# Optimization experiments

Measured on AMD Instinct MI355X. Metric: run time of the kernel, lower is better.

## Reference

```python
import math
import jax, jax.numpy as jnp
import numpy as np

HEADS = 8
DIM_HEAD = 32
DIM = 128
EPS_LN = 1e-5
EPS_NORM = 1e-12


def setup_inputs() -> dict:
    key = jax.random.key(0)
    ks = jax.random.split(key, 4)
    inner = HEADS * DIM_HEAD  # 256
    x = jax.random.normal(ks[0], (1, DIM, 16, 64, 64), dtype=jnp.float32)
    g = jnp.ones((1, DIM, 1, 1, 1), dtype=jnp.float32)
    b = jnp.zeros((1, DIM, 1, 1, 1), dtype=jnp.float32)
    w_qkv = jax.random.normal(ks[1], (3 * inner, DIM), dtype=jnp.float32) * 0.05
    w_out = jax.random.normal(ks[2], (DIM, inner), dtype=jnp.float32) * 0.05
    b_out = jnp.zeros((DIM,), dtype=jnp.float32)
    return {"x": x, "g": g, "b": b, "w_qkv": w_qkv, "w_out": w_out, "b_out": b_out}


def _l2norm_ch(t):
    # F.normalize(t, dim=1): divide by max(||t||_2, eps) along channel axis
    n = jnp.sqrt(jnp.sum(t * t, axis=1, keepdims=True))
    return t / jnp.maximum(n, EPS_NORM)


def _gather_axis(t, idx, axis):
    # t: [bh, c, D, H, W]; idx: [bh, kk]; gather along spatial `axis`
    shape = list(t.shape)
    shape[axis] = idx.shape[1]
    ix = idx.reshape((idx.shape[0],) + (1,) * (axis - 1) + (idx.shape[1],) + (1,) * (4 - axis))
    ix = jnp.broadcast_to(ix, shape)
    return jnp.take_along_axis(t, ix, axis=axis)


def _dpsa_forward(x, g, b, w_qkv, w_out, b_out):
    bsz, c, D, H, W = x.shape
    kd = int(math.ceil(D ** 0.5))
    kh = int(math.ceil(H ** 0.5))
    kw = int(math.ceil(W ** 0.5))

    # ChanLayerNorm3d (biased variance over channel dim)
    mean = jnp.mean(x, axis=1, keepdims=True)
    var = jnp.var(x, axis=1, keepdims=True)
    xn = (x - mean) / jnp.sqrt(var + EPS_LN) * g + b

    # 1x1x1 conv to qkv (no bias)
    qkv = jnp.einsum('oc,bcdhw->bodhw', w_qkv, xn)
    inner = HEADS * DIM_HEAD
    q, k, v = qkv[:, :inner], qkv[:, inner:2 * inner], qkv[:, 2 * inner:]

    def fold(t):  # b (i c) d h w -> (b i) c d h w
        return t.reshape(bsz * HEADS, DIM_HEAD, D, H, W)
    q, k, v = fold(q), fold(k), fold(v)
    D0, H0, W0 = D, H, W

    q = _l2norm_ch(q)
    k = _l2norm_ch(k)
    q_abs = jnp.abs(q)

    # depth pruning
    if kd < D:
        q_probe = q_abs.sum(axis=(3, 4))                 # [bh, c, D]
        k_probe = jnp.abs(k).sum(axis=(3, 4))            # [bh, c, D]
        score = jnp.einsum('bcd,bcd->bd', q_probe, k_probe)
        _, idx = jax.lax.top_k(score, kd)
        k = _gather_axis(k, idx, 2)
        v = _gather_axis(v, idx, 2)
        D = kd
    # height pruning
    if kh < H:
        q_probe = q_abs.sum(axis=(2, 4))                 # [bh, c, H]
        k_probe = jnp.abs(k).sum(axis=(2, 4))            # [bh, c, H]
        score = jnp.einsum('bch,bch->bh', q_probe, k_probe)
        _, idx = jax.lax.top_k(score, kh)
        k = _gather_axis(k, idx, 3)
        v = _gather_axis(v, idx, 3)
        H = kh
    # width pruning
    if kw < W:
        q_probe = q_abs.sum(axis=(2, 3))                 # [bh, c, W]
        k_probe = jnp.abs(k).sum(axis=(2, 3))            # [bh, c, W]
        score = jnp.einsum('bcw,bcw->bw', q_probe, k_probe)
        _, idx = jax.lax.top_k(score, kw)
        k = _gather_axis(k, idx, 4)
        v = _gather_axis(v, idx, 4)
        W = kw

    def flat(t):  # b c d h w -> b (dhw) c
        return t.reshape(t.shape[0], t.shape[1], -1).transpose(0, 2, 1)
    qf, kf, vf = flat(q), flat(k), flat(v)

    sim = jnp.einsum('bic,bjc->bij', qf, kf)  # note: original applies no scale
    attn = jax.nn.softmax(sim, axis=-1)
    out_flat = jnp.einsum('bij,bjc->bic', attn, vf)  # [bh, N, c]

    # faithful to torch .view: raw row-major reinterpretation
    out = out_flat.reshape(bsz * HEADS, DIM_HEAD, D0, H0, W0)
    out = out.reshape(bsz, HEADS * DIM_HEAD, D0, H0, W0)
    return jnp.einsum('oc,bcdhw->bodhw', w_out, out) + b_out[None, :, None, None, None]


def reference(x, g, b, w_qkv, w_out, b_out):
    return _dpsa_forward(x, g, b, w_qkv, w_out, b_out)
```

## Files before the change

### kernel.cpp

```cpp
#include <hip/hip_runtime.h>
#include <math.h>

#define P_TOT 65536
#define CH    128
#define NHEAD 8
#define KD    4
#define KH    8
#define KW    8
#define NJ    256

typedef unsigned short u16;
typedef unsigned int   u32;
typedef __attribute__((ext_vector_type(8))) short frag8;
typedef __attribute__((ext_vector_type(4))) float f32x4;

__device__ inline u16 bf16r(float a) {
    u32 ua = __float_as_uint(a);
    return (u16)((ua + 0x7fff + ((ua >> 16) & 1)) >> 16);
}
__device__ inline float bf16f(u16 h) {
    return __uint_as_float(((u32)h) << 16);
}
__device__ inline u32 packhl(float v) {
    u16 hh = bf16r(v);
    u16 ll = bf16r(v - bf16f(hh));
    return (u32)hh | ((u32)ll << 16);
}

__global__ __launch_bounds__(256) void k_ln(const float* __restrict__ x,
                                            const float* __restrict__ g,
                                            const float* __restrict__ b,
                                            u16* __restrict__ xn_hi,
                                            u16* __restrict__ xn_lo) {
    __shared__ u32 buf[64 * 131];
    __shared__ float red[8 * 64];
    __shared__ float stat[2 * 64];
    float* xt = (float*)buf;
    int t  = threadIdx.x;
    int p0 = blockIdx.x * 64;
    #pragma unroll
    for (int r = 0; r < 8; ++r) {
        int id = t + 256 * r;
        int c = id >> 4, q4 = id & 15;
        *(float4*)(xt + c * 64 + q4 * 4) =
            *(const float4*)(x + (size_t)c * P_TOT + p0 + q4 * 4);
    }
    __syncthreads();
    int pp = t & 63, part = t >> 6;
    float sum = 0.f, ssq = 0.f;
    for (int ci = 0; ci < 32; ++ci) {
        float v = xt[(part * 32 + ci) * 64 + pp];
        sum += v; ssq += v * v;
    }
    red[part * 64 + pp] = sum;
    red[256 + part * 64 + pp] = ssq;
    __syncthreads();
    if (t < 64) {
        float s = red[t] + red[64 + t] + red[128 + t] + red[192 + t];
        float q = red[256 + t] + red[320 + t] + red[384 + t] + red[448 + t];
        float mean = s * (1.f / CH);
        float var  = q * (1.f / CH) - mean * mean;
        stat[t] = mean;
        stat[64 + t] = 1.f / sqrtf(var + 1e-5f);
    }
    __syncthreads();
    float mean = stat[pp], inv = stat[64 + pp];
    u32 pk[32];
    for (int ci = 0; ci < 32; ++ci) {
        int c = part * 32 + ci;
        float v  = xt[c * 64 + pp];
        float xn = (v - mean) * inv * g[c] + b[c];
        pk[ci] = packhl(xn);
    }
    __syncthreads();
    u32* tr = buf;
    for (int ci = 0; ci < 32; ++ci)
        tr[pp * 131 + part * 32 + ci] = pk[ci];
    __syncthreads();
    #pragma unroll
    for (int r = 0; r < 8; ++r) {
        int id = t + 256 * r;
        int pr = id >> 5, ch = id & 31;
        const u32* srcp = tr + pr * 131 + ch * 4;
        u32 v0 = srcp[0], v1 = srcp[1], v2 = srcp[2], v3 = srcp[3];
        uint2 hv, lv;
        hv.x = __builtin_amdgcn_perm(v1, v0, 0x05040100);
        hv.y = __builtin_amdgcn_perm(v3, v2, 0x05040100);
        lv.x = __builtin_amdgcn_perm(v1, v0, 0x07060302);
        lv.y = __builtin_amdgcn_perm(v3, v2, 0x07060302);
        size_t off = (size_t)(p0 + pr) * 128 + ch * 4;
        *(uint2*)(xn_hi + off) = hv;
        *(uint2*)(xn_lo + off) = lv;
    }
}

__global__ __launch_bounds__(256) void k_wsplit(const float* __restrict__ wqkv,
                                                const float* __restrict__ wout,
                                                u16* __restrict__ w_hi,
                                                u16* __restrict__ w_lo,
                                                u16* __restrict__ w2_hi,
                                                u16* __restrict__ w2_lo,
                                                float* __restrict__ zbuf) {
    int id = blockIdx.x * 256 + threadIdx.x;
    if (id < 40960) zbuf[id] = 0.f;
    if (id < 65536) {
        float v = wqkv[id];
        u16 hh = bf16r(v);
        w_hi[id] = hh; w_lo[id] = bf16r(v - bf16f(hh));
    } else {
        int j = id - 65536;
        float v = wout[j];
        u16 hh = bf16r(v);
        w2_hi[j] = hh; w2_lo[j] = bf16r(v - bf16f(hh));
    }
}

__global__ __launch_bounds__(256) void k_gemm_qkv(const u16* __restrict__ xn_hi,
                                                  const u16* __restrict__ xn_lo,
                                                  const u16* __restrict__ w_hi,
                                                  const u16* __restrict__ w_lo,
                                                  float* __restrict__ qk,
                                                  u16* __restrict__ qT,
                                                  float* __restrict__ pd,
                                                  float* __restrict__ pdh,
                                                  float* __restrict__ qph,
                                                  float* __restrict__ qpw) {
    __shared__ u16 smem[4 * 128 * 64];
    u16* a_hi = smem;
    u16* a_lo = smem + 8192;
    u16* b_hi = smem + 16384;
    u16* b_lo = smem + 24576;
    int t    = threadIdx.x;
    int lane = t & 63, wave = t >> 6;
    int wp = wave & 1, wo = wave >> 1;
    int m = lane & 15, quad = lane >> 4;
    int p0 = blockIdx.x * 128;
    int o0 = blockIdx.y * 128;
    f32x4 acc[4][4] = {};
    for (int k0 = 0; k0 < 128; k0 += 64) {
        __syncthreads();
        #pragma unroll
        for (int r = 0; r < 4; ++r) {
            int id  = t + 256 * r;
            int row = id >> 3, gg = id & 7;
            int gs  = gg ^ (row & 7);
            int dst = row * 64 + gg * 8;
            size_t sa = (size_t)(p0 + row) * 128 + k0 + gs * 8;
            size_t sb = (size_t)(o0 + row) * 128 + k0 + gs * 8;
            *(uint4*)(a_hi + dst) = *(const uint4*)(xn_hi + sa);
            *(uint4*)(a_lo + dst) = *(const uint4*)(xn_lo + sa);
            *(uint4*)(b_hi + dst) = *(const uint4*)(w_hi + sb);
            *(uint4*)(b_lo + dst) = *(const uint4*)(w_lo + sb);
        }
        __syncthreads();
        #pragma unroll
        for (int ks = 0; ks < 2; ++ks) {
            frag8 ah[4], al[4], bh[4], bl[4];
            #pragma unroll
            for (int i = 0; i < 4; ++i) {
                int row = wp * 64 + i * 16 + m;
                int gg  = (ks * 4 + quad) ^ (row & 7);
                ah[i] = *(const frag8*)(a_hi + row * 64 + gg * 8);
                al[i] = *(const frag8*)(a_lo + row * 64 + gg * 8);
            }
            #pragma unroll
            for (int j = 0; j < 4; ++j) {
                int row = wo * 64 + j * 16 + m;
                int gg  = (ks * 4 + quad) ^ (row & 7);
                bh[j] = *(const frag8*)(b_hi + row * 64 + gg * 8);
                bl[j] = *(const frag8*)(b_lo + row * 64 + gg * 8);
            }
            #pragma unroll
            for (int i = 0; i < 4; ++i)
                #pragma unroll
                for (int j = 0; j < 4; ++j) {
                    acc[i][j] = __builtin_amdgcn_mfma_f32_16x16x32_bf16(ah[i], bh[j], acc[i][j], 0, 0, 0);
                    acc[i][j] = __builtin_amdgcn_mfma_f32_16x16x32_bf16(ah[i], bl[j], acc[i][j], 0, 0, 0);
                    acc[i][j] = __builtin_amdgcn_mfma_f32_16x16x32_bf16(al[i], bh[j], acc[i][j], 0, 0, 0);
                }
        }
    }
    #pragma unroll
    for (int i = 0; i < 4; ++i) {
        #pragma unroll
        for (int jg = 0; jg < 2; ++jg) {
            f32x4 s;
            #pragma unroll
            for (int r = 0; r < 4; ++r)
                s[r] = acc[i][2 * jg][r] * acc[i][2 * jg][r]
                     + acc[i][2 * jg + 1][r] * acc[i][2 * jg + 1][r];
            #pragma unroll
            for (int mask = 1; mask <= 8; mask <<= 1) {
                s[0] += __shfl_xor(s[0], mask, 64);
                s[1] += __shfl_xor(s[1], mask, 64);
                s[2] += __shfl_xor(s[2], mask, 64);
                s[3] += __shfl_xor(s[3], mask, 64);
            }
            #pragma unroll
            for (int r = 0; r < 4; ++r) {
                float inv = 1.f / fmaxf(sqrtf(s[r]), 1e-12f);
                acc[i][2 * jg][r]     *= inv;
                acc[i][2 * jg + 1][r] *= inv;
            }
        }
    }
    int pb = blockIdx.x;
    int d  = pb >> 5;
    int hh = (2 * pb + wp) & 63;
    bool isQ = (o0 < 256);
    {
        float sj[4];
        #pragma unroll
        for (int j = 0; j < 4; ++j) {
            float s = 0.f;
            #pragma unroll
            for (int i = 0; i < 4; ++i)
                #pragma unroll
                for (int r = 0; r < 4; ++r)
                    s += fabsf(acc[i][j][r]);
            sj[j] = s;
        }
        #pragma unroll
        for (int j = 0; j < 4; ++j) {
            sj[j] += __shfl_xor(sj[j], 16, 64);
            sj[j] += __shfl_xor(sj[j], 32, 64);
        }
        if (quad == 0) {
            #pragma unroll
            for (int j = 0; j < 4; ++j) {
                int o = o0 + wo * 64 + j * 16 + m;
                atomicAdd(pd + o * 16 + d, sj[j]);
                if (isQ) atomicAdd(qph + o * 64 + hh, sj[j]);
                else     pdh[((size_t)o * 16 + d) * 64 + hh] = sj[j];
            }
        }
    }
    if (isQ) {
        float* qw = (float*)smem;
        __syncthreads();
        if (wp == 0) {
            #pragma unroll
            for (int j = 0; j < 4; ++j) {
                int ol = wo * 64 + j * 16 + m;
                #pragma unroll
                for (int i = 0; i < 4; ++i)
                    #pragma unroll
                    for (int r = 0; r < 4; ++r)
                        qw[(i * 16 + quad * 4 + r) * 132 + ol] = fabsf(acc[i][j][r]);
            }
        }
        __syncthreads();
        if (wp == 1) {
            #pragma unroll
            for (int j = 0; j < 4; ++j) {
                int ol = wo * 64 + j * 16 + m;
                #pragma unroll
                for (int i = 0; i < 4; ++i)
                    #pragma unroll
                    for (int r = 0; r < 4; ++r)
                        qw[(i * 16 + quad * 4 + r) * 132 + ol] += fabsf(acc[i][j][r]);
            }
        }
        __syncthreads();
        #pragma unroll
        for (int ri = 0; ri < 32; ++ri) {
            int id = t + 256 * ri;
            int ol = id >> 6, w = id & 63;
            atomicAdd(qpw + (size_t)(o0 + ol) * 64 + w, qw[w * 132 + ol]);
        }
    } else {
        #pragma unroll
        for (int i = 0; i < 4; ++i) {
            int p = p0 + wp * 64 + i * 16 + quad * 4;
            #pragma unroll
            for (int j = 0; j < 4; ++j) {
                int o = o0 + wo * 64 + j * 16 + m;
                float4 v;
                v.x = acc[i][j][0]; v.y = acc[i][j][1];
                v.z = acc[i][j][2]; v.w = acc[i][j][3];
                *(float4*)(qk + (size_t)o * P_TOT + p) = v;
            }
        }
    }
    if (isQ) {
        __syncthreads();
        u16* qtb = smem;
        #pragma unroll
        for (int i = 0; i < 4; ++i)
            #pragma unroll
            for (int j = 0; j < 4; ++j) {
                int grp = wo * 2 + (j >> 1);
                int c   = (j & 1) * 16 + m;
                #pragma unroll
                for (int r = 0; r < 4; ++r) {
                    int pl = wp * 64 + i * 16 + quad * 4 + r;
                    qtb[grp * 5120 + pl * 40 + c] = bf16r(acc[i][j][r]);
                }
            }
        __syncthreads();
        int gbase = o0 >> 5;
        #pragma unroll
        for (int ri = 0; ri < 8; ++ri) {
            int id = t + 256 * ri;
            int grp = id >> 9, rem = id & 511;
            int pl = rem >> 2, cq = rem & 3;
            uint4 v = *(const uint4*)(qtb + grp * 5120 + pl * 40 + cq * 8);
            *(uint4*)(qT + ((size_t)(gbase + grp) * P_TOT + p0 + pl) * 32 + cq * 8) = v;
        }
    }
}

__global__ __launch_bounds__(64) void k_topk_d(const float* __restrict__ pd,
                                               int* __restrict__ idx_d) {
    int h = blockIdx.x, t = threadIdx.x;
    __shared__ float sc[16];
    if (t < 16) {
        float s = 0.f;
        for (int c = 0; c < 32; ++c)
            s += pd[(h * 32 + c) * 16 + t] * pd[(256 + h * 32 + c) * 16 + t];
        sc[t] = s;
    }
    __syncthreads();
    if (t == 0) {
        bool used[16] = {};
        for (int r = 0; r < KD; ++r) {
            int best = 0; float bv = -1e30f;
            for (int i = 0; i < 16; ++i)
                if (!used[i] && sc[i] > bv) { bv = sc[i]; best = i; }
            used[best] = true;
            idx_d[h * KD + r] = best;
        }
    }
}

__global__ __launch_bounds__(256) void k_topk_h(const float* __restrict__ qph,
                                                const float* __restrict__ pdh,
                                                const int* __restrict__ idx_d,
                                                int* __restrict__ idx_h) {
    int h = blockIdx.x, t = threadIdx.x;
    int tq = t & 63, cg = t >> 6;
    __shared__ float sc2[4][64];
    __shared__ float sc[64];
    int ds[KD];
    #pragma unroll
    for (int i = 0; i < KD; ++i) ds[i] = idx_d[h * KD + i];
    float partial = 0.f;
    for (int ci = 0; ci < 8; ++ci) {
        int c  = cg * 8 + ci;
        int oq = h * 32 + c, ok = 256 + h * 32 + c;
        float qp = qph[oq * 64 + tq];
        float kp = 0.f;
        #pragma unroll
        for (int i = 0; i < KD; ++i) kp += pdh[(ok * 16 + ds[i]) * 64 + tq];
        partial += qp * kp;
    }
    sc2[cg][tq] = partial;
    __syncthreads();
    if (t < 64) sc[t] = sc2[0][t] + sc2[1][t] + sc2[2][t] + sc2[3][t];
    __syncthreads();
    if (t == 0) {
        bool used[64] = {};
        for (int r = 0; r < KH; ++r) {
            int best = 0; float bv = -1e30f;
            for (int i = 0; i < 64; ++i)
                if (!used[i] && sc[i] > bv) { bv = sc[i]; best = i; }
            used[best] = true;
            idx_h[h * KH + r] = best;
        }
    }
}

__global__ __launch_bounds__(64) void k_probe_w(const float* __restrict__ qk,
                                                const int* __restrict__ idx_d,
                                                const int* __restrict__ idx_h,
                                                float* __restrict__ kpw) {
    int o2 = blockIdx.x;
    int w  = threadIdx.x;
    int h  = o2 >> 5;
    const float* src = qk + (256 + o2) * P_TOT;
    float s = 0.f;
    for (int i = 0; i < KD; ++i) {
        int pb = idx_d[h * KD + i] * 4096;
        for (int j = 0; j < KH; ++j)
            s += fabsf(src[pb + idx_h[h * KH + j] * 64 + w]);
    }
    kpw[o2 * 64 + w] = s;
}

__global__ __launch_bounds__(256) void k_topk_w(const float* __restrict__ qpw,
                                                const float* __restrict__ kpw,
                                                int* __restrict__ idx_w) {
    int h = blockIdx.x, t = threadIdx.x;
    int tq = t & 63, cg = t >> 6;
    __shared__ float sc2[4][64];
    __shared__ float sc[64];
    float partial = 0.f;
    for (int ci = 0; ci < 8; ++ci) {
        int c  = cg * 8 + ci;
        int oq = h * 32 + c;
        partial += qpw[oq * 64 + tq] * kpw[(h * 32 + c) * 64 + tq];
    }
    sc2[cg][tq] = partial;
    __syncthreads();
    if (t < 64) sc[t] = sc2[0][t] + sc2[1][t] + sc2[2][t] + sc2[3][t];
    __syncthreads();
    if (t == 0) {
        bool used[64] = {};
        for (int r = 0; r < KW; ++r) {
            int best = 0; float bv = -1e30f;
            for (int i = 0; i < 64; ++i)
                if (!used[i] && sc[i] > bv) { bv = sc[i]; best = i; }
            used[best] = true;
            idx_w[h * KW + r] = best;
        }
    }
}

__global__ __launch_bounds__(64) void k_gather(const float* __restrict__ qk,
                                               const u16* __restrict__ xn_hi,
                                               const u16* __restrict__ xn_lo,
                                               const float* __restrict__ wqkv,
                                               const int* __restrict__ idx_d,
                                               const int* __restrict__ idx_h,
                                               const int* __restrict__ idx_w,
                                               u16* __restrict__ kb,
                                               u16* __restrict__ vT) {
    int h  = blockIdx.x;
    int jb = blockIdx.y;
    int t  = threadIdx.x;
    int j  = jb * 2 + (t >> 5);
    int c  = t & 31;
    int di = j >> 6, hi = (j >> 3) & 7, wi = j & 7;
    int p  = idx_d[h * KD + di] * 4096 + idx_h[h * KH + hi] * 64 + idx_w[h * KW + wi];
    kb[(h * NJ + j) * 32 + c] = bf16r(qk[(256 + h * 32 + c) * P_TOT + p]);
    const float* wr = wqkv + (512 + h * 32 + c) * CH;
    const u16* xh = xn_hi + (size_t)p * 128;
    const u16* xl = xn_lo + (size_t)p * 128;
    float acc = 0.f;
    for (int cc = 0; cc < CH; ++cc) {
        float v = bf16f(xh[cc]) + bf16f(xl[cc]);
        acc += wr[cc] * v;
    }
    int pos = (j & 0xE0) | ((j & 0x0C) << 1) | ((j & 0x10) >> 2) | (j & 3);
    vT[((size_t)h * 32 + c) * NJ + pos] = bf16r(acc);
}

__device__ inline frag8 mk_frag(uint2 a, uint2 b) {
    union { u32 u[4]; frag8 f; } v;
    v.u[0] = a.x; v.u[1] = a.y; v.u[2] = b.x; v.u[3] = b.y;
    return v.f;
}

__global__ __launch_bounds__(256) void k_attn(const u16* __restrict__ qT,
                                              const u16* __restrict__ kb,
                                              const u16* __restrict__ vT,
                                              u32* __restrict__ attn_pk) {
    __shared__ u16 sK[256 * 32];
    __shared__ u16 sV[32 * 264];
    int h    = blockIdx.x >> 8;
    int pc   = blockIdx.x & 255;
    int wave = threadIdx.x >> 6;
    int lane = threadIdx.x & 63;
    int m    = lane & 15;
    int quad = lane >> 4;
    int t    = threadIdx.x;

    int qbase = pc * 256 + wave * 64;
    frag8 bq[4];
    #pragma unroll
    for (int i = 0; i < 4; ++i)
        bq[i] = *(const frag8*)(qT + ((size_t)h * P_TOT + qbase + i * 16 + m) * 32 + quad * 8);

    const uint4* kg  = (const uint4*)(kb + (size_t)h * NJ * 32);
    uint4*       sKg = (uint4*)sK;
    #pragma unroll
    for (int r = 0; r < 4; ++r)
        sKg[t + 256 * r] = kg[t + 256 * r];
    const uint4* vg = (const uint4*)(vT + (size_t)h * 32 * NJ);
    #pragma unroll
    for (int r = 0; r < 4; ++r) {
        int g2 = t + 256 * r;
        int row = g2 >> 5, col = g2 & 31;
        *(uint4*)(sV + row * 264 + col * 8) = vg[g2];
    }
    __syncthreads();

    f32x4 zero = {0.f, 0.f, 0.f, 0.f};
    #pragma unroll
    for (int tile = 0; tile < 4; ++tile) {
        int p = qbase + tile * 16 + m;
        float den = 0.f;
        uint2 pk[16];
        #pragma unroll
        for (int tt = 0; tt < 16; ++tt) {
            frag8 ak = *(const frag8*)(sK + (tt * 16 + m) * 32 + quad * 8);
            f32x4 st = __builtin_amdgcn_mfma_f32_16x16x32_bf16(ak, bq[tile], zero, 0, 0, 0);
            float e0 = __expf(st[0]);
            float e1 = __expf(st[1]);
            float e2 = __expf(st[2]);
            float e3 = __expf(st[3]);
            den += (e0 + e1) + (e2 + e3);
            pk[tt].x = __builtin_amdgcn_perm(__float_as_uint(e1), __float_as_uint(e0), 0x07060302);
            pk[tt].y = __builtin_amdgcn_perm(__float_as_uint(e3), __float_as_uint(e2), 0x07060302);
        }
        den += __shfl_xor(den, 16, 64);
        den += __shfl_xor(den, 32, 64);

        f32x4 a0e = zero, a0o = zero, a1e = zero, a1o = zero;
        #pragma unroll
        for (int jc = 0; jc < 8; jc += 2) {
            frag8 bp0  = mk_frag(pk[2 * jc],     pk[2 * jc + 1]);
            frag8 bp1  = mk_frag(pk[2 * jc + 2], pk[2 * jc + 3]);
            frag8 av00 = *(const frag8*)(sV + m * 264 + jc * 32 + quad * 8);
            frag8 av01 = *(const frag8*)(sV + m * 264 + (jc + 1) * 32 + quad * 8);
            frag8 av10 = *(const frag8*)(sV + (16 + m) * 264 + jc * 32 + quad * 8);
            frag8 av11 = *(const frag8*)(sV + (16 + m) * 264 + (jc + 1) * 32 + quad * 8);
            a0e = __builtin_amdgcn_mfma_f32_16x16x32_bf16(av00, bp0, a0e, 0, 0, 0);
            a0o = __builtin_amdgcn_mfma_f32_16x16x32_bf16(av01, bp1, a0o, 0, 0, 0);
            a1e = __builtin_amdgcn_mfma_f32_16x16x32_bf16(av10, bp0, a1e, 0, 0, 0);
            a1o = __builtin_amdgcn_mfma_f32_16x16x32_bf16(av11, bp1, a1o, 0, 0, 0);
        }
        f32x4 acc0 = a0e + a0o;
        f32x4 acc1 = a1e + a1o;
        float inv = 1.f / den;
        size_t base = ((size_t)(h * 32 + (p >> 11))) * P_TOT + (size_t)(p & 2047) * 32;
        uint4 o0, o1;
        o0.x = packhl(acc0[0] * inv); o0.y = packhl(acc0[1] * inv);
        o0.z = packhl(acc0[2] * inv); o0.w = packhl(acc0[3] * inv);
        o1.x = packhl(acc1[0] * inv); o1.y = packhl(acc1[1] * inv);
        o1.z = packhl(acc1[2] * inv); o1.w = packhl(acc1[3] * inv);
        *(uint4*)(attn_pk + base + quad * 4)      = o0;
        *(uint4*)(attn_pk + base + 16 + quad * 4) = o1;
    }
}

__global__ __launch_bounds__(256) void k_gemm_out(const u32* __restrict__ attn_pk,
                                                  const u16* __restrict__ w2_hi,
                                                  const u16* __restrict__ w2_lo,
                                                  const float* __restrict__ bout,
                                                  float* __restrict__ out) {
    __shared__ u16 a_hi[128 * 64], a_lo[128 * 64];
    __shared__ u16 b_hi[128 * 64], b_lo[128 * 64];
    int t    = threadIdx.x;
    int lane = t & 63, wave = t >> 6;
    int wq = wave & 1, wo = wave >> 1;
    int m = lane & 15, quad = lane >> 4;
    int q0 = blockIdx.x * 128;
    f32x4 acc[4][4] = {};
    for (int k0 = 0; k0 < 256; k0 += 64) {
        __syncthreads();
        #pragma unroll
        for (int r = 0; r < 4; ++r) {
            int id = t + 256 * r;
            int qq = id & 127, gsel = id >> 7;
            u32 pkk[8];
            #pragma unroll
            for (int e = 0; e < 8; ++e)
                pkk[e] = attn_pk[(size_t)(k0 + gsel * 8 + e) * P_TOT + q0 + qq];
            u32 hi4[4], lo4[4];
            #pragma unroll
            for (int e = 0; e < 4; ++e) {
                hi4[e] = __builtin_amdgcn_perm(pkk[2*e+1], pkk[2*e], 0x05040100);
                lo4[e] = __builtin_amdgcn_perm(pkk[2*e+1], pkk[2*e], 0x07060302);
            }
            int go = (gsel ^ (qq & 7)) * 8;
            *(uint4*)(a_hi + qq * 64 + go) = *(uint4*)hi4;
            *(uint4*)(a_lo + qq * 64 + go) = *(uint4*)lo4;
        }
        #pragma unroll
        for (int r = 0; r < 4; ++r) {
            int id  = t + 256 * r;
            int row = id >> 3, gg = id & 7;
            int go  = (gg ^ (row & 7)) * 8;
            *(uint4*)(b_hi + row * 64 + go) =
                *(const uint4*)(w2_hi + (size_t)row * 256 + k0 + gg * 8);
            *(uint4*)(b_lo + row * 64 + go) =
                *(const uint4*)(w2_lo + (size_t)row * 256 + k0 + gg * 8);
        }
        __syncthreads();
        #pragma unroll
        for (int ks = 0; ks < 2; ++ks) {
            frag8 ah[4], al[4], bh[4], bl[4];
            #pragma unroll
            for (int i = 0; i < 4; ++i) {
                int row = wq * 64 + i * 16 + m;
                int gg  = (ks * 4 + quad) ^ (row & 7);
                ah[i] = *(const frag8*)(a_hi + row * 64 + gg * 8);
                al[i] = *(const frag8*)(a_lo + row * 64 + gg * 8);
            }
            #pragma unroll
            for (int j = 0; j < 4; ++j) {
                int row = wo * 64 + j * 16 + m;
                int gg  = (ks * 4 + quad) ^ (row & 7);
                bh[j] = *(const frag8*)(b_hi + row * 64 + gg * 8);
                bl[j] = *(const frag8*)(b_lo + row * 64 + gg * 8);
            }
            #pragma unroll
            for (int i = 0; i < 4; ++i)
                #pragma unroll
                for (int j = 0; j < 4; ++j) {
                    acc[i][j] = __builtin_amdgcn_mfma_f32_16x16x32_bf16(ah[i], bh[j], acc[i][j], 0, 0, 0);
                    acc[i][j] = __builtin_amdgcn_mfma_f32_16x16x32_bf16(ah[i], bl[j], acc[i][j], 0, 0, 0);
                    acc[i][j] = __builtin_amdgcn_mfma_f32_16x16x32_bf16(al[i], bh[j], acc[i][j], 0, 0, 0);
                }
        }
    }
    #pragma unroll
    for (int j = 0; j < 4; ++j) {
        int o = wo * 64 + j * 16 + m;
        float bv = bout[o];
        #pragma unroll
        for (int i = 0; i < 4; ++i) {
            int q = q0 + wq * 64 + i * 16 + quad * 4;
            float4 v;
            v.x = acc[i][j][0] + bv; v.y = acc[i][j][1] + bv;
            v.z = acc[i][j][2] + bv; v.w = acc[i][j][3] + bv;
            *(float4*)(out + (size_t)o * P_TOT + q) = v;
        }
    }
}

extern "C" void kernel_launch(void* const* d_in, const int* in_sizes, int n_in,
                              void* d_out, int out_size, void* d_ws, size_t ws_size,
                              hipStream_t stream) {
    const float* x    = (const float*)d_in[0];
    const float* g    = (const float*)d_in[1];
    const float* b    = (const float*)d_in[2];
    const float* wqkv = (const float*)d_in[3];
    const float* wout = (const float*)d_in[4];
    const float* bout = (const float*)d_in[5];
    float* out = (float*)d_out;
    float* ws  = (float*)d_ws;

    u16*   xn_hi = (u16*)ws;
    u16*   xn_lo = xn_hi + (size_t)128 * P_TOT;
    float* qk   = ws + 8388608;
    u32*   attn_pk = (u32*)(qk + 256 * P_TOT);
    float* aux  = ws + 41943040;
    float* pd    = aux;
    float* qph   = pd + 8192;
    float* qpw   = qph + 16384;
    float* pdh   = qpw + 16384;
    float* kpw   = pdh + 524288;
    int*   idx_d = (int*)(kpw + 16384);
    int*   idx_h = idx_d + 32;
    int*   idx_w = idx_h + 64;
    u16*   kb    = (u16*)(idx_w + 64);
    u16*   vT    = kb + 8 * NJ * 32;
    u16*   qT    = vT + 8 * 32 * NJ;
    u16*   w_hi  = qT + (size_t)8 * P_TOT * 32;
    u16*   w_lo  = w_hi + 512 * 128;
    u16*   w2_hi = w_lo + 512 * 128;
    u16*   w2_lo = w2_hi + 128 * 256;

    k_ln<<<1024, 256, 0, stream>>>(x, g, b, xn_hi, xn_lo);
    k_wsplit<<<384, 256, 0, stream>>>(wqkv, wout, w_hi, w_lo, w2_hi, w2_lo, pd);
    k_gemm_qkv<<<dim3(512, 4), 256, 0, stream>>>(xn_hi, xn_lo, w_hi, w_lo,
                                                 qk, qT, pd, pdh, qph, qpw);
    k_topk_d<<<8, 64, 0, stream>>>(pd, idx_d);
    k_topk_h<<<8, 256, 0, stream>>>(qph, pdh, idx_d, idx_h);
    k_probe_w<<<256, 64, 0, stream>>>(qk, idx_d, idx_h, kpw);
    k_topk_w<<<8, 256, 0, stream>>>(qpw, kpw, idx_w);
    k_gather<<<dim3(8, 128), 64, 0, stream>>>(qk, xn_hi, xn_lo, wqkv,
                                              idx_d, idx_h, idx_w, kb, vT);
    k_attn<<<2048, 256, 0, stream>>>(qT, kb, vT, attn_pk);
    k_gemm_out<<<512, 256, 0, stream>>>(attn_pk, w2_hi, w2_lo, bout, out);
}
```

Baseline: 408.0 us.

## Replace global atomic probe reductions with per-block partials and separate reduce kernels

The QKV GEMM epilogue no longer issues atomicAdds for the depth, height and width probe sums. It writes per-block partials instead: the per-(o,d,h) values already stored in pdh, plus a new per-block width-partial buffer placed in the q region of qk, which is never written because q goes to qT. Two small kernels then reduce these into pd and qpw, and k_topk_h sums the q height probe directly from pdh. This removes atomic contention and the zero-init, at the cost of two extra launches and extra partial-buffer traffic. The shared-memory stride also changes from 132 to 129.

```diff
diff --git a/kernel.cpp b/kernel.cpp
--- a/kernel.cpp
+++ b/kernel.cpp
@@ -99,10 +99,8 @@
                                                 u16* __restrict__ w_hi,
                                                 u16* __restrict__ w_lo,
                                                 u16* __restrict__ w2_hi,
-                                                u16* __restrict__ w2_lo,
-                                                float* __restrict__ zbuf) {
+                                                u16* __restrict__ w2_lo) {
     int id = blockIdx.x * 256 + threadIdx.x;
-    if (id < 40960) zbuf[id] = 0.f;
     if (id < 65536) {
         float v = wqkv[id];
         u16 hh = bf16r(v);
@@ -121,10 +119,8 @@
                                                   const u16* __restrict__ w_lo,
                                                   float* __restrict__ qk,
                                                   u16* __restrict__ qT,
-                                                  float* __restrict__ pd,
                                                   float* __restrict__ pdh,
-                                                  float* __restrict__ qph,
-                                                  float* __restrict__ qpw) {
+                                                  float* __restrict__ qpwp) {
     __shared__ u16 smem[4 * 128 * 64];
     u16* a_hi = smem;
     u16* a_lo = smem + 8192;
@@ -229,9 +225,7 @@
             #pragma unroll
             for (int j = 0; j < 4; ++j) {
                 int o = o0 + wo * 64 + j * 16 + m;
-                atomicAdd(pd + o * 16 + d, sj[j]);
-                if (isQ) atomicAdd(qph + o * 64 + hh, sj[j]);
-                else     pdh[((size_t)o * 16 + d) * 64 + hh] = sj[j];
+                pdh[((size_t)o * 16 + d) * 64 + hh] = sj[j];
             }
         }
     }
@@ -246,7 +240,7 @@
                 for (int i = 0; i < 4; ++i)
                     #pragma unroll
                     for (int r = 0; r < 4; ++r)
-                        qw[(i * 16 + quad * 4 + r) * 132 + ol] = fabsf(acc[i][j][r]);
+                        qw[(i * 16 + quad * 4 + r) * 129 + ol] = fabsf(acc[i][j][r]);
             }
         }
         __syncthreads();
@@ -258,15 +252,16 @@
                 for (int i = 0; i < 4; ++i)
                     #pragma unroll
                     for (int r = 0; r < 4; ++r)
-                        qw[(i * 16 + quad * 4 + r) * 132 + ol] += fabsf(acc[i][j][r]);
-            }
-        }
-        __syncthreads();
+                        qw[(i * 16 + quad * 4 + r) * 129 + ol] += fabsf(acc[i][j][r]);
+            }
+        }
+        __syncthreads();
+        float* dstp = qpwp + ((size_t)(blockIdx.y * 512 + pb)) * 8192;
         #pragma unroll
         for (int ri = 0; ri < 32; ++ri) {
             int id = t + 256 * ri;
             int ol = id >> 6, w = id & 63;
-            atomicAdd(qpw + (size_t)(o0 + ol) * 64 + w, qw[w * 132 + ol]);
+            dstp[id] = qw[w * 129 + ol];
         }
     } else {
         #pragma unroll
@@ -308,6 +303,32 @@
             *(uint4*)(qT + ((size_t)(gbase + grp) * P_TOT + p0 + pl) * 32 + cq * 8) = v;
         }
     }
+}
+
+__global__ __launch_bounds__(256) void k_pd(const float* __restrict__ pdh,
+                                            float* __restrict__ pd) {
+    int gid = blockIdx.x * 256 + threadIdx.x;
+    const float* src = pdh + (size_t)gid * 64;
+    float s = 0.f;
+    #pragma unroll
+    for (int h = 0; h < 64; ++h) s += src[h];
+    pd[gid] = s;
+}
+
+__global__ __launch_bounds__(256) void k_qpw(const float* __restrict__ qpwp,
+                                             float* __restrict__ qpw) {
+    int o = blockIdx.x;
+    int t = threadIdx.x;
+    int w = t & 63, sub = t >> 6;
+    int y = o >> 7, ol = o & 127;
+    __shared__ float red[256];
+    float s = 0.f;
+    #pragma unroll 8
+    for (int pb = sub * 128; pb < sub * 128 + 128; ++pb)
+        s += qpwp[((size_t)(y * 512 + pb)) * 8192 + ol * 64 + w];
+    red[t] = s;
+    __syncthreads();
+    if (t < 64) qpw[o * 64 + w] = red[w] + red[64 + w] + red[128 + w] + red[192 + w];
 }
 
 __global__ __launch_bounds__(64) void k_topk_d(const float* __restrict__ pd,
@@ -333,8 +354,7 @@
     }
 }
 
-__global__ __launch_bounds__(256) void k_topk_h(const float* __restrict__ qph,
-                                                const float* __restrict__ pdh,
+__global__ __launch_bounds__(256) void k_topk_h(const float* __restrict__ pdh,
                                                 const int* __restrict__ idx_d,
                                                 int* __restrict__ idx_h) {
     int h = blockIdx.x, t = threadIdx.x;
@@ -348,10 +368,13 @@
     for (int ci = 0; ci < 8; ++ci) {
         int c  = cg * 8 + ci;
         int oq = h * 32 + c, ok = 256 + h * 32 + c;
-        float qp = qph[oq * 64 + tq];
+        float qp = 0.f;
+        #pragma unroll
+        for (int dq = 0; dq < 16; ++dq)
+            qp += pdh[((size_t)oq * 16 + dq) * 64 + tq];
         float kp = 0.f;
         #pragma unroll
-        for (int i = 0; i < KD; ++i) kp += pdh[(ok * 16 + ds[i]) * 64 + tq];
+        for (int i = 0; i < KD; ++i) kp += pdh[((size_t)ok * 16 + ds[i]) * 64 + tq];
         partial += qp * kp;
     }
     sc2[cg][tq] = partial;
@@ -377,7 +400,7 @@
     int o2 = blockIdx.x;
     int w  = threadIdx.x;
     int h  = o2 >> 5;
-    const float* src = qk + (256 + o2) * P_TOT;
+    const float* src = qk + (size_t)(256 + o2) * P_TOT;
     float s = 0.f;
     for (int i = 0; i < KD; ++i) {
         int pb = idx_d[h * KD + i] * 4096;
@@ -432,7 +455,7 @@
     int c  = t & 31;
     int di = j >> 6, hi = (j >> 3) & 7, wi = j & 7;
     int p  = idx_d[h * KD + di] * 4096 + idx_h[h * KH + hi] * 64 + idx_w[h * KW + wi];
-    kb[(h * NJ + j) * 32 + c] = bf16r(qk[(256 + h * 32 + c) * P_TOT + p]);
+    kb[(h * NJ + j) * 32 + c] = bf16r(qk[(size_t)(256 + h * 32 + c) * P_TOT + p]);
     const float* wr = wqkv + (512 + h * 32 + c) * CH;
     const u16* xh = xn_hi + (size_t)p * 128;
     const u16* xl = xn_lo + (size_t)p * 128;
@@ -635,11 +658,11 @@
     u16*   xn_hi = (u16*)ws;
     u16*   xn_lo = xn_hi + (size_t)128 * P_TOT;
     float* qk   = ws + 8388608;
-    u32*   attn_pk = (u32*)(qk + 256 * P_TOT);
+    float* qpwp = qk;
+    u32*   attn_pk = (u32*)(qk + (size_t)256 * P_TOT);
     float* aux  = ws + 41943040;
     float* pd    = aux;
-    float* qph   = pd + 8192;
-    float* qpw   = qph + 16384;
+    float* qpw   = pd + 8192;
     float* pdh   = qpw + 16384;
     float* kpw   = pdh + 524288;
     int*   idx_d = (int*)(kpw + 16384);
@@ -654,11 +677,13 @@
     u16*   w2_lo = w2_hi + 128 * 256;
 
     k_ln<<<1024, 256, 0, stream>>>(x, g, b, xn_hi, xn_lo);
-    k_wsplit<<<384, 256, 0, stream>>>(wqkv, wout, w_hi, w_lo, w2_hi, w2_lo, pd);
+    k_wsplit<<<384, 256, 0, stream>>>(wqkv, wout, w_hi, w_lo, w2_hi, w2_lo);
     k_gemm_qkv<<<dim3(512, 4), 256, 0, stream>>>(xn_hi, xn_lo, w_hi, w_lo,
-                                                 qk, qT, pd, pdh, qph, qpw);
+                                                 qk, qT, pdh, qpwp);
+    k_pd<<<32, 256, 0, stream>>>(pdh, pd);
+    k_qpw<<<256, 256, 0, stream>>>(qpwp, qpw);
     k_topk_d<<<8, 64, 0, stream>>>(pd, idx_d);
-    k_topk_h<<<8, 256, 0, stream>>>(qph, pdh, idx_d, idx_h);
+    k_topk_h<<<8, 256, 0, stream>>>(pdh, idx_d, idx_h);
     k_probe_w<<<256, 64, 0, stream>>>(qk, idx_d, idx_h, kpw);
     k_topk_w<<<8, 256, 0, stream>>>(qpw, kpw, idx_w);
     k_gather<<<dim3(8, 128), 64, 0, stream>>>(qk, xn_hi, xn_lo, wqkv,
```

Result: faster. 330.4 us, median of 3 (-19.0%).
